# Performance work log

Hardware: AMD Instinct MI355X
Metric: run time of the kernel (lower is better)

## Reference

```python
import jax, jax.numpy as jnp
import numpy as np

N = 50000      # amino-acid nodes
DIN = 64       # input feature dim
DH = 64        # hidden dim (= GAT out_feats per head)
H = 4          # attention heads
E_RES, E_SEQ, E_KNN = 400000, 100000, 400000
EPS = 1e-5


def setup_inputs() -> dict:
    key = jax.random.key(0)
    ks = iter(jax.random.split(key, 32))
    def nrm(shape, scale=0.1):
        return jax.random.normal(next(ks), shape, dtype=jnp.float32) * scale
    def edges(E):
        s = jax.random.randint(next(ks), (E,), 0, N, dtype=jnp.int32)
        d = jax.random.randint(next(ks), (E,), 0, N, dtype=jnp.int32)
        return s, d
    x = nrm((N, DIN), 1.0)
    src_res, dst_res = edges(E_RES)
    src_seq, dst_seq = edges(E_SEQ)
    src_knn, dst_knn = edges(E_KNN)
    inp = dict(x=x, src_res=src_res, dst_res=dst_res, src_seq=src_seq,
               dst_seq=dst_seq, src_knn=src_knn, dst_knn=dst_knn)
    # layer 0 (in=DIN), layer 1 (in=DH): per-relation stacked GAT params
    inp.update(W0=nrm((3, DIN, H * DH)), al0=nrm((3, H, DH)), ar0=nrm((3, H, DH)),
               b0=nrm((3, H * DH)), rW0=nrm((3, DIN, H * DH)))
    inp.update(W1=nrm((3, DH, H * DH)), al1=nrm((3, H, DH)), ar1=nrm((3, H, DH)),
               b1=nrm((3, H * DH)), rW1=nrm((3, DH, H * DH)))
    inp.update(fcW0=nrm((DH, DH)), fcb0=nrm((DH,)), fcW1=nrm((DH, DH)), fcb1=nrm((DH,)))
    inp.update(g0=jnp.ones((DIN,), jnp.float32), be0=jnp.zeros((DIN,), jnp.float32),
               g1=jnp.ones((DH,), jnp.float32), be1=jnp.zeros((DH,), jnp.float32))
    return inp


def _bn(x, g, b):
    mu = jnp.mean(x, axis=0)
    var = jnp.mean((x - mu) ** 2, axis=0)
    return (x - mu) * jax.lax.rsqrt(var + EPS) * g + b


def _gat(h, src, dst, W, al, ar, bias, rW):
    # DGL GATConv (feat_drop off in eval, residual=True via res_fc Linear, bias)
    n = h.shape[0]
    fs = (h @ W).reshape(n, H, DH)                    # [N,H,D]
    el = jnp.sum(fs * al, axis=-1)                    # [N,H]
    er = jnp.sum(fs * ar, axis=-1)
    e = jax.nn.leaky_relu(el[src] + er[dst], 0.2)     # [E,H]
    m = jax.ops.segment_max(e, dst, num_segments=n)
    a = jnp.exp(e - m[dst])
    s = jax.ops.segment_sum(a, dst, num_segments=n)
    alpha = a / s[dst]                                # edge-softmax per dst/head
    rst = jax.ops.segment_sum(alpha[:, :, None] * fs[src], dst, num_segments=n)
    return rst + (h @ rW).reshape(n, H, DH) + bias.reshape(1, H, DH)


def _layer(x, edges, W, al, ar, b, rW, fcW, fcb, g, be):
    x = _bn(x, g, be)
    h = jnp.zeros((x.shape[0], H, DH), x.dtype)
    for r, (s_, d_) in enumerate(edges):              # 3 relation types, summed
        h = h + _gat(x, s_, d_, W[r], al[r], ar[r], b[r], rW[r])
    x = jnp.mean(h, axis=1)                           # mean over heads
    return jax.nn.relu(x @ fcW + fcb)


def reference(x, src_res, dst_res, src_seq, dst_seq, src_knn, dst_knn,
              W0, al0, ar0, b0, rW0, W1, al1, ar1, b1, rW1,
              fcW0, fcb0, fcW1, fcb1, g0, be0, g1, be1):
    edges = [(src_res, dst_res), (src_seq, dst_seq), (src_knn, dst_knn)]
    x = _layer(x, edges, W0, al0, ar0, b0, rW0, fcW0, fcb0, g0, be0)
    x = _layer(x, edges, W1, al1, ar1, b1, rW1, fcW1, fcb1, g1, be1)
    return x
```

## Files before the change

kernel.cpp:

```cpp
#include <hip/hip_runtime.h>
#include <math.h>

#define NN    50000
#define DD    64
#define HH    4
#define E_RES 400000
#define E_SEQ 100000
#define E_KNN 400000
#define ETOT  (E_RES+E_SEQ+E_KNN)
#define RPS   (NN + 4)
#define NBLK  ((NN+255)/256)
#define KTOT  864
#define CTPS  (ETOT + 32)
#define NBUK  98
#define TBUK  (3*NBUK)
#define EPB   4096
#define PABLK ((ETOT+EPB-1)/EPB)
#define FBLK  (NN/16)
#define ECB2  ((3*NN + 31)/32)
#define LZS   810

typedef __attribute__((ext_vector_type(8))) short short8;
typedef __attribute__((ext_vector_type(4))) float floatx4;

__device__ inline unsigned short f2bf(float f){
  union{float f; unsigned u;} v; v.f=f;
  unsigned r = v.u + 0x7FFF + ((v.u>>16)&1);
  return (unsigned short)(r>>16);
}
__device__ inline float bf2f(unsigned short u){
  union{unsigned u; float f;} v; v.u=(unsigned)u<<16; return v.f;
}

__global__ void __launch_bounds__(256)
k_bucketcnt(const int* __restrict__ d0, const int* __restrict__ d1,
            const int* __restrict__ d2, int* __restrict__ bcnt){
  __shared__ int cnt[TBUK];
  int t = threadIdx.x;
  for(int i=t;i<TBUK;i+=256) cnt[i]=0;
  __syncthreads();
  int ebase = blockIdx.x*EPB;
  #pragma unroll
  for(int j=0;j<16;j++){
    int i = ebase + j*256 + t;
    int d, r;
    if(i < E_RES){ d=d0[i]; r=0; }
    else if(i < E_RES+E_SEQ){ d=d1[i-E_RES]; r=1; }
    else if(i < ETOT){ d=d2[i-E_RES-E_SEQ]; r=2; }
    else continue;
    atomicAdd(&cnt[r*NBUK + (d>>9)], 1);
  }
  __syncthreads();
  for(int i=t;i<TBUK;i+=256){ int c=cnt[i]; if(c) atomicAdd(&bcnt[i], c); }
}

__global__ void k_bucketscan(const int* __restrict__ bcnt,
                             int* __restrict__ bbase, int* __restrict__ bcur){
  __shared__ int sh[TBUK];
  int t = threadIdx.x;
  if(t < 64){
    int carry = 0;
    for(int c=0;c<5;c++){
      int idx = c*64 + t;
      int v = (idx < TBUK) ? bcnt[idx] : 0;
      int inc = v;
      for(int off=1; off<64; off<<=1){ int n=__shfl_up(inc, off, 64); if(t>=off) inc+=n; }
      if(idx < TBUK) sh[idx] = carry + inc - v;
      carry += __shfl(inc, 63, 64);
    }
  }
  __syncthreads();
  if(t < TBUK){ bbase[t] = sh[t]; bcur[t] = sh[t]; }
  if(t == 0) bbase[TBUK] = ETOT;
}

__global__ void __launch_bounds__(256)
k_partA(const int* __restrict__ s0, const int* __restrict__ d0,
        const int* __restrict__ s1, const int* __restrict__ d1,
        const int* __restrict__ s2, const int* __restrict__ d2,
        int* __restrict__ bcur, unsigned* __restrict__ pairs){
  __shared__ int cnt[TBUK];
  __shared__ int gb[TBUK];
  int t = threadIdx.x;
  for(int i=t;i<TBUK;i+=256) cnt[i]=0;
  __syncthreads();
  int ebase = blockIdx.x*EPB;
  unsigned meta[16], pk[16];
  #pragma unroll
  for(int j=0;j<16;j++){
    int i = ebase + j*256 + t;
    int s, d, r;
    if(i < E_RES){ s=s0[i]; d=d0[i]; r=0; }
    else if(i < E_RES+E_SEQ){ int k=i-E_RES; s=s1[k]; d=d1[k]; r=1; }
    else if(i < ETOT){ int k=i-E_RES-E_SEQ; s=s2[k]; d=d2[k]; r=2; }
    else { meta[j]=0xFFFFFFFFu; continue; }
    int bk = r*NBUK + (d>>9);
    int rk = atomicAdd(&cnt[bk], 1);
    meta[j] = ((unsigned)bk<<16) | (unsigned)rk;
    pk[j]   = ((unsigned)(d&511)<<16) | (unsigned)s;
  }
  __syncthreads();
  for(int i=t;i<TBUK;i+=256){ int c=cnt[i]; gb[i] = c ? atomicAdd(&bcur[i], c) : 0; }
  __syncthreads();
  #pragma unroll
  for(int j=0;j<16;j++){
    unsigned mt = meta[j];
    if(mt != 0xFFFFFFFFu)
      pairs[gb[mt>>16] + (mt & 0xFFFFu)] = pk[j];
  }
}

__global__ void __launch_bounds__(256)
k_partB(const unsigned* __restrict__ pairs, const int* __restrict__ bbase,
        int* __restrict__ rowptr, int* __restrict__ csr){
  int bb = blockIdx.x, r = bb / NBUK, b = bb - r*NBUK;
  int dbase = b*512, dmax = min(512, NN - dbase);
  int off = (r==0)?0:(r==1)?E_RES:(E_RES+E_SEQ);
  __shared__ int hist[512];
  __shared__ int curs[513];
  int t = threadIdx.x;
  hist[t]=0; hist[256+t]=0;
  __syncthreads();
  int beg = bbase[bb], end = bbase[bb+1];
  for(int i=beg+t; i<end; i+=256) atomicAdd(&hist[pairs[i]>>16], 1);
  __syncthreads();
  if(t < 64){
    int carry = 0;
    for(int c=0;c<8;c++){
      int v = hist[c*64+t];
      int inc = v;
      for(int o2=1; o2<64; o2<<=1){ int n=__shfl_up(inc, o2, 64); if(t>=o2) inc+=n; }
      curs[c*64+t] = (beg - off) + carry + inc - v;
      carry += __shfl(inc, 63, 64);
    }
    if(t==0) curs[512] = end - off;
  }
  __syncthreads();
  int* rp = rowptr + r*RPS + dbase;
  for(int i=t; i<=dmax; i+=256) rp[i] = curs[i];
  __syncthreads();
  for(int i=beg+t; i<end; i+=256){
    unsigned p = pairs[i];
    int pos = atomicAdd(&curs[p>>16], 1);
    csr[off + pos] = (int)(p & 0xFFFFu);
  }
}

__global__ void k_bnstats(const float* __restrict__ x, float* __restrict__ stats,
                          unsigned short* __restrict__ Abf){
  __shared__ float sh[512];
  int t = threadIdx.x, col = t & 63, rg = t >> 6;
  float s=0.f, q=0.f;
  for(int row = blockIdx.x*4 + rg; row < NN; row += gridDim.x*4){
    float v = x[(size_t)row*64 + col]; s += v; q += v*v;
    Abf[(size_t)row*64 + col] = f2bf(v);
  }
  sh[t]=s; sh[256+t]=q; __syncthreads();
  if(rg==0){
    s = sh[col]+sh[64+col]+sh[128+col]+sh[192+col];
    q = sh[256+col]+sh[320+col]+sh[384+col]+sh[448+col];
    atomicAdd(&stats[col], s); atomicAdd(&stats[64+col], q);
  }
}

__global__ void __launch_bounds__(256)
k_prep3(const float* __restrict__ stats, const float* __restrict__ g,
        const float* __restrict__ be, const float* __restrict__ W,
        const float* __restrict__ al, const float* __restrict__ ar,
        const float* __restrict__ b, const float* __restrict__ rW,
        const float* __restrict__ fcW, const float* __restrict__ fcb,
        float* __restrict__ wbufF){
  __shared__ float scale[64], shift[64];
  int t = threadIdx.x;
  if(t<64){
    float mu  = stats[t]*(1.0f/NN);
    float var = stats[64+t]*(1.0f/NN) - mu*mu;
    float sc  = g[t]*rsqrtf(var + 1e-5f);
    scale[t]=sc; shift[t]=be[t]-mu*sc;
  }
  __syncthreads();
  char* wb = (char*)wbufF;
  unsigned short* Wf = (unsigned short*)wbufF;
  float* biasF = (float*)(wb + 110592);
  int bid = blockIdx.x;
  if(bid < 52){
    __shared__ float fcWs[4096];
    for(int i=t;i<4096;i+=256) fcWs[i]=fcW[i];
    __syncthreads();
    int j = bid*16 + (t>>4);
    int cg = (t&15)*4;
    float Wrow[64];
    if(j < 64){
      for(int d=0; d<64; d++){
        float w=0.f;
        for(int r=0;r<3;r++)
          #pragma unroll
          for(int h=0;h<4;h++)
            w += rW[((size_t)(r*64+j))*256 + h*64 + d];
        Wrow[d] = scale[j]*0.25f*w;
      }
    } else {
      int jj = j-64;
      int r = jj>>8, dc = jj&255, h = dc&3, c = dc>>2;
      const float* Wp = W + ((size_t)(r*64+c))*256 + h*64;
      float sc = 0.25f*scale[c];
      #pragma unroll
      for(int d=0; d<64; d++) Wrow[d] = sc*Wp[d];
    }
    #pragma unroll
    for(int cc=0; cc<4; cc++){
      int col = cg+cc;
      float acc=0.f;
      #pragma unroll
      for(int d=0; d<64; d++) acc += Wrow[d]*fcWs[d*64+col];
      Wf[(size_t)col*KTOT + j] = f2bf(acc);
    }
  } else if(bid < 58){
    int wv = (bid-52)*4 + (t>>6);
    int r = wv >> 3, cc = wv & 7, h = cc & 3, k = t & 63;
    const float* av = ((cc>=4)?ar:al) + (r*HH+h)*64;
    const float* Wk = W + ((size_t)(r*64+k))*256 + h*64;
    float w=0.f;
    for(int d2=0; d2<64; d2++) w += Wk[d2]*av[d2];
    float* WelR = (float*)(wb + 110848 + r*2080);
    WelR[cc*64 + k] = scale[k]*w;
    float bp = shift[k]*w;
    for(int off=32; off; off>>=1) bp += __shfl_down(bp, off, 64);
    if(k==0) (WelR + 512)[cc] = bp;
  } else {
    __shared__ float S[3][64];
    __shared__ float BH[64];
    if(t<192){
      int r=t>>6, d=t&63;
      float s=0.f;
      #pragma unroll
      for(int h=0;h<4;h++){
        const float* Wp = W + (size_t)(r*64)*256 + h*64 + d;
        for(int k=0;k<64;k++) s += shift[k]*Wp[(size_t)k*256];
      }
      S[r][d]=0.25f*s;
    } else {
      int d = t-192;
      float s=0.f;
      for(int k=0;k<64;k++){
        float w=0.f;
        for(int r=0;r<3;r++)
          #pragma unroll
          for(int h=0;h<4;h++)
            w += rW[((size_t)(r*64+k))*256 + h*64 + d];
        s += shift[k]*0.25f*w;
      }
      float bb=0.f;
      for(int r=0;r<3;r++)
        #pragma unroll
        for(int h=0;h<4;h++) bb += b[r*256 + h*64 + d];
      BH[d] = s + 0.25f*bb;
    }
    __syncthreads();
    if(t<192){
      int r=t>>6, col=t&63;
      float acc=0.f;
      for(int d=0;d<64;d++) acc += S[r][d]*fcW[d*64+col];
      Wf[(size_t)col*KTOT + 832 + r] = f2bf(acc);
    } else {
      int col=t-192;
      float acc=0.f;
      for(int d=0;d<64;d++) acc += BH[d]*fcW[d*64+col];
      biasF[col] = acc + fcb[col];
    }
    if(t<64){
      for(int j=835;j<KTOT;j++) Wf[(size_t)t*KTOT + j] = 0;
    }
  }
}

__global__ void __launch_bounds__(256)
k_el3(const float* __restrict__ A, const float* __restrict__ wbufF,
      float* __restrict__ EL){
  int r = blockIdx.x / NBLK;
  const char* wb = (const char*)wbufF;
  const float* Wel = (const float*)(wb + 110848 + r*2080);
  const float* biasE = Wel + 512;
  float* ELr = EL + (size_t)r*NN*8;
  __shared__ float sw[512];
  __shared__ float sb[8];
  int t = threadIdx.x;
  sw[t]=Wel[t]; sw[256+t]=Wel[256+t];
  if(t<8) sb[t]=biasE[t];
  __syncthreads();
  int n = (blockIdx.x % NBLK)*256 + t;
  if(n>=NN) return;
  float acc[8];
  #pragma unroll
  for(int c=0;c<8;c++) acc[c]=sb[c];
  const float4* Ar = (const float4*)(A + (size_t)n*64);
  #pragma unroll
  for(int kq=0;kq<16;kq++){
    float4 a = Ar[kq];
    #pragma unroll
    for(int c=0;c<8;c++){
      const float* w = sw + c*64 + kq*4;
      acc[c] += a.x*w[0] + a.y*w[1] + a.z*w[2] + a.w*w[3];
    }
  }
  ((float4*)ELr)[n*2]   = make_float4(acc[0],acc[1],acc[2],acc[3]);
  ((float4*)ELr)[n*2+1] = make_float4(acc[4],acc[5],acc[6],acc[7]);
}

#define EC_GATHER(ii, E0,E1,E2,E3) { \
    int src_ = cs[ii]; \
    float4 el_ = ((const float4*)ELr)[src_*2]; \
    E0=el_.x+er.x; E1=el_.y+er.y; E2=el_.z+er.z; E3=el_.w+er.w; \
    E0 = E0>0.f? E0 : 0.2f*E0; \
    E1 = E1>0.f? E1 : 0.2f*E1; \
    E2 = E2>0.f? E2 : 0.2f*E2; \
    E3 = E3>0.f? E3 : 0.2f*E3; }
#define EC_ACC(E0,E1,E2,E3) { \
    float n0_=fmaxf(m0,E0); s0=s0*__expf(m0-n0_)+__expf(E0-n0_); m0=n0_; \
    float n1_=fmaxf(m1,E1); s1=s1*__expf(m1-n1_)+__expf(E1-n1_); m1=n1_; \
    float n2_=fmaxf(m2,E2); s2=s2*__expf(m2-n2_)+__expf(E2-n2_); m2=n2_; \
    float n3_=fmaxf(m3,E3); s3=s3*__expf(m3-n3_)+__expf(E3-n3_); m3=n3_; }
#define EC_COMB(o) { \
    float om_,os_,nm_; \
    om_=__shfl_xor(m0,o,64); os_=__shfl_xor(s0,o,64); \
    nm_=fmaxf(m0,om_); s0=s0*__expf(m0-nm_)+os_*__expf(om_-nm_); m0=nm_; \
    om_=__shfl_xor(m1,o,64); os_=__shfl_xor(s1,o,64); \
    nm_=fmaxf(m1,om_); s1=s1*__expf(m1-nm_)+os_*__expf(om_-nm_); m1=nm_; \
    om_=__shfl_xor(m2,o,64); os_=__shfl_xor(s2,o,64); \
    nm_=fmaxf(m2,om_); s2=s2*__expf(m2-nm_)+os_*__expf(om_-nm_); m2=nm_; \
    om_=__shfl_xor(m3,o,64); os_=__shfl_xor(s3,o,64); \
    nm_=fmaxf(m3,om_); s3=s3*__expf(m3-nm_)+os_*__expf(om_-nm_); m3=nm_; }
#define EC_STORE(ii, E0,E1,E2,E3) { \
    t0[ii]=f2bf(__expf(E0-m0)*r0); t1[ii]=f2bf(__expf(E1-m1)*r1); \
    t2[ii]=f2bf(__expf(E2-m2)*r2); t3[ii]=f2bf(__expf(E3-m3)*r3); }

__global__ void __launch_bounds__(256)
k_edgecoef3(const float* __restrict__ EL, const int* __restrict__ rowptr,
            const int* __restrict__ csr, unsigned short* __restrict__ coefT){
  int item = blockIdx.x*32 + (threadIdx.x>>3);
  int sl = threadIdx.x & 7;
  if(item >= 3*NN) return;
  int r = item / NN, n = item - r*NN;
  const float* ELr = EL + (size_t)r*NN*8;
  const int* rp = rowptr + r*RPS;
  int off = (r==0)?0:(r==1)?E_RES:(E_RES+E_SEQ);
  const int* cs = csr + off;
  unsigned short* t0 = coefT + off;
  unsigned short* t1 = coefT + (size_t)CTPS + off;
  unsigned short* t2 = coefT + (size_t)2*CTPS + off;
  unsigned short* t3 = coefT + (size_t)3*CTPS + off;
  int beg = rp[n], end = rp[n+1];
  if(end <= beg) return;
  const float4 er = ((const float4*)ELr)[n*2+1];
  float m0=-1e30f,m1=-1e30f,m2=-1e30f,m3=-1e30f;
  float s0=0.f,s1=0.f,s2=0.f,s3=0.f;
  int i0 = beg + sl, i1 = i0 + 8, i2 = i0 + 16, i3 = i0 + 24;
  bool h0 = i0 < end, h1 = i1 < end, h2 = i2 < end, h3 = i3 < end;
  float a0=0.f,a1=0.f,a2=0.f,a3=0.f;
  float b0=0.f,b1=0.f,b2=0.f,b3=0.f;
  float c0=0.f,c1=0.f,c2=0.f,c3=0.f;
  float d0=0.f,d1=0.f,d2=0.f,d3=0.f;
  if(h0){ EC_GATHER(i0, a0,a1,a2,a3); EC_ACC(a0,a1,a2,a3); }
  if(h1){ EC_GATHER(i1, b0,b1,b2,b3); EC_ACC(b0,b1,b2,b3); }
  if(h2){ EC_GATHER(i2, c0,c1,c2,c3); EC_ACC(c0,c1,c2,c3); }
  if(h3){ EC_GATHER(i3, d0,d1,d2,d3); EC_ACC(d0,d1,d2,d3); }
  for(int i = i0 + 32; i < end; i += 8){
    float e0,e1,e2,e3;
    EC_GATHER(i, e0,e1,e2,e3);
    EC_ACC(e0,e1,e2,e3);
  }
  EC_COMB(1) EC_COMB(2) EC_COMB(4)
  float r0=1.f/s0, r1=1.f/s1, r2=1.f/s2, r3=1.f/s3;
  if(h0) EC_STORE(i0, a0,a1,a2,a3);
  if(h1) EC_STORE(i1, b0,b1,b2,b3);
  if(h2) EC_STORE(i2, c0,c1,c2,c3);
  if(h3) EC_STORE(i3, d0,d1,d2,d3);
  for(int i = i0 + 32; i < end; i += 8){
    float e0,e1,e2,e3;
    EC_GATHER(i, e0,e1,e2,e3);
    EC_STORE(i, e0,e1,e2,e3);
  }
}

__global__ void __launch_bounds__(256)
k_fused(const unsigned short* __restrict__ Abf, const int* __restrict__ rowptr,
        const int* __restrict__ csr, const unsigned short* __restrict__ coefT,
        const float* __restrict__ wbufF, float* __restrict__ out,
        unsigned short* __restrict__ Abf2, float* __restrict__ stats, int dostats){
  __shared__ unsigned short Zl[16*LZS];
  const unsigned short* Wf = (const unsigned short*)wbufF;
  const float* biasF = (const float*)((const char*)wbufF + 110592);
  int t = threadIdx.x, wv = t>>6, lane = t&63, m = lane&15, kq = lane>>4;
  int nb = blockIdx.x*16;
  int n4 = nb + wv*4;
  int nn = m>>2, h = m&3;
  for(int i=t; i<512; i+=256){ int nd=i>>5, j=i&31; if(j<29) Zl[nd*LZS+771+j]=0; }
  for(int r=0;r<3;r++){
    const int* rp = rowptr + r*RPS;
    int off = (r==0)?0:(r==1)?E_RES:(E_RES+E_SEQ);
    const int* cs = csr + off;
    const unsigned short* cT = coefT + (size_t)h*CTPS + off;
    int rpn  = rp[n4+nn];
    int rpn1 = rp[n4+nn+1];
    unsigned dg = (unsigned)(rpn1 - rpn);
    int beg = __shfl(rpn, 0, 64);
    int end = __shfl(rpn1, 15, 64);
    floatx4 acc0={0.f,0.f,0.f,0.f};
    floatx4 acc1={0.f,0.f,0.f,0.f};
    floatx4 acc2={0.f,0.f,0.f,0.f};
    floatx4 acc3={0.f,0.f,0.f,0.f};
    for(int eb = (beg & ~31); eb < end; eb += 32){
      int p0 = eb + kq*8;
      union { uint4 q; short8 v; } af;
      af.q = *(const uint4*)(cT + p0);
      int qd = p0 - rpn;
      unsigned w0 = (((unsigned)(qd+0)<dg)?0x0000FFFFu:0u) | (((unsigned)(qd+1)<dg)?0xFFFF0000u:0u);
      unsigned w1 = (((unsigned)(qd+2)<dg)?0x0000FFFFu:0u) | (((unsigned)(qd+3)<dg)?0xFFFF0000u:0u);
      unsigned w2 = (((unsigned)(qd+4)<dg)?0x0000FFFFu:0u) | (((unsigned)(qd+5)<dg)?0xFFFF0000u:0u);
      unsigned w3 = (((unsigned)(qd+6)<dg)?0x0000FFFFu:0u) | (((unsigned)(qd+7)<dg)?0xFFFF0000u:0u);
      af.q.x &= w0; af.q.y &= w1; af.q.z &= w2; af.q.w &= w3;
      const int* csp = cs + p0;
      int s0=csp[0],s1=csp[1],s2=csp[2],s3=csp[3],s4=csp[4],s5=csp[5],s6=csp[6],s7=csp[7];
      const unsigned short* q0 = Abf + ((size_t)s0<<6) + m;
      const unsigned short* q1 = Abf + ((size_t)s1<<6) + m;
      const unsigned short* q2 = Abf + ((size_t)s2<<6) + m;
      const unsigned short* q3 = Abf + ((size_t)s3<<6) + m;
      const unsigned short* q4 = Abf + ((size_t)s4<<6) + m;
      const unsigned short* q5 = Abf + ((size_t)s5<<6) + m;
      const unsigned short* q6 = Abf + ((size_t)s6<<6) + m;
      const unsigned short* q7 = Abf + ((size_t)s7<<6) + m;
      union { unsigned u[4]; short8 v; } b0,b1,b2,b3;
      b0.u[0]=(unsigned)q0[0] |((unsigned)q1[0]<<16);
      b0.u[1]=(unsigned)q2[0] |((unsigned)q3[0]<<16);
      b0.u[2]=(unsigned)q4[0] |((unsigned)q5[0]<<16);
      b0.u[3]=(unsigned)q6[0] |((unsigned)q7[0]<<16);
      b1.u[0]=(unsigned)q0[16]|((unsigned)q1[16]<<16);
      b1.u[1]=(unsigned)q2[16]|((unsigned)q3[16]<<16);
      b1.u[2]=(unsigned)q4[16]|((unsigned)q5[16]<<16);
      b1.u[3]=(unsigned)q6[16]|((unsigned)q7[16]<<16);
      b2.u[0]=(unsigned)q0[32]|((unsigned)q1[32]<<16);
      b2.u[1]=(unsigned)q2[32]|((unsigned)q3[32]<<16);
      b2.u[2]=(unsigned)q4[32]|((unsigned)q5[32]<<16);
      b2.u[3]=(unsigned)q6[32]|((unsigned)q7[32]<<16);
      b3.u[0]=(unsigned)q0[48]|((unsigned)q1[48]<<16);
      b3.u[1]=(unsigned)q2[48]|((unsigned)q3[48]<<16);
      b3.u[2]=(unsigned)q4[48]|((unsigned)q5[48]<<16);
      b3.u[3]=(unsigned)q6[48]|((unsigned)q7[48]<<16);
      acc0 = __builtin_amdgcn_mfma_f32_16x16x32_bf16(af.v, b0.v, acc0, 0,0,0);
      acc1 = __builtin_amdgcn_mfma_f32_16x16x32_bf16(af.v, b1.v, acc1, 0,0,0);
      acc2 = __builtin_amdgcn_mfma_f32_16x16x32_bf16(af.v, b2.v, acc2, 0,0,0);
      acc3 = __builtin_amdgcn_mfma_f32_16x16x32_bf16(af.v, b3.v, acc3, 0,0,0);
    }
    unsigned short* zrow = Zl + (wv*4+kq)*LZS + r*256 + m*4;
    ushort4 o;
    o.x=f2bf(acc0[0]); o.y=f2bf(acc0[1]); o.z=f2bf(acc0[2]); o.w=f2bf(acc0[3]);
    *(ushort4*)(zrow)       = o;
    o.x=f2bf(acc1[0]); o.y=f2bf(acc1[1]); o.z=f2bf(acc1[2]); o.w=f2bf(acc1[3]);
    *(ushort4*)(zrow + 64)  = o;
    o.x=f2bf(acc2[0]); o.y=f2bf(acc2[1]); o.z=f2bf(acc2[2]); o.w=f2bf(acc2[3]);
    *(ushort4*)(zrow + 128) = o;
    o.x=f2bf(acc3[0]); o.y=f2bf(acc3[1]); o.z=f2bf(acc3[2]); o.w=f2bf(acc3[3]);
    *(ushort4*)(zrow + 192) = o;
    int degk = __shfl((int)dg, kq<<2, 64);
    if(m==0)
      Zl[(wv*4+kq)*LZS + 768 + r] = degk>0 ? (unsigned short)0x3F80 : (unsigned short)0;
  }
  __syncthreads();
  floatx4 acc = {0.f,0.f,0.f,0.f};
  const unsigned short* Arow = Abf + (size_t)(nb+m)*64;
  const unsigned short* Zrow = Zl + m*LZS;
  #pragma unroll
  for(int kb=0; kb<27; kb++){
    short8 a;
    if(kb<2) a = *(const short8*)(Arow + kb*32 + kq*8);
    else     a = *(const short8*)(Zrow + (kb-2)*32 + kq*8);
    short8 b = *(const short8*)(Wf + (size_t)(wv*16+m)*KTOT + kb*32 + kq*8);
    acc = __builtin_amdgcn_mfma_f32_16x16x32_bf16(a, b, acc, 0,0,0);
  }
  int col = wv*16 + m;
  float bb = biasF[col];
  float sv=0.f, qv=0.f;
  #pragma unroll
  for(int ri=0; ri<4; ri++){
    int ro = nb + kq*4 + ri;
    float v = fmaxf(acc[ri] + bb, 0.f);
    out[(size_t)ro*64 + col] = v;
    if(dostats){
      Abf2[(size_t)ro*64 + col] = f2bf(v);
      sv += v; qv += v*v;
    }
  }
  if(dostats){
    sv += __shfl_xor(sv, 16, 64); qv += __shfl_xor(qv, 16, 64);
    sv += __shfl_xor(sv, 32, 64); qv += __shfl_xor(qv, 32, 64);
    if(kq==0){ atomicAdd(&stats[col], sv); atomicAdd(&stats[64+col], qv); }
  }
}

extern "C" void kernel_launch(void* const* d_in, const int* in_sizes, int n_in,
                              void* d_out, int out_size, void* d_ws, size_t ws_size,
                              hipStream_t stream){
  const float* x      =(const float*)d_in[0];
  const int* src_res  =(const int*)d_in[1];
  const int* dst_res  =(const int*)d_in[2];
  const int* src_seq  =(const int*)d_in[3];
  const int* dst_seq  =(const int*)d_in[4];
  const int* src_knn  =(const int*)d_in[5];
  const int* dst_knn  =(const int*)d_in[6];
  const float* W0 =(const float*)d_in[7];
  const float* al0=(const float*)d_in[8];
  const float* ar0=(const float*)d_in[9];
  const float* b0 =(const float*)d_in[10];
  const float* rW0=(const float*)d_in[11];
  const float* W1 =(const float*)d_in[12];
  const float* al1=(const float*)d_in[13];
  const float* ar1=(const float*)d_in[14];
  const float* b1 =(const float*)d_in[15];
  const float* rW1=(const float*)d_in[16];
  const float* fcW0=(const float*)d_in[17];
  const float* fcb0=(const float*)d_in[18];
  const float* fcW1=(const float*)d_in[19];
  const float* fcb1=(const float*)d_in[20];
  const float* g0 =(const float*)d_in[21];
  const float* be0=(const float*)d_in[22];
  const float* g1 =(const float*)d_in[23];
  const float* be1=(const float*)d_in[24];

  char* ws=(char*)d_ws;
  int*   bcnt   =(int*)  (ws+0);
  int*   bbase  =(int*)  (ws+4096);
  float* stats0 =(float*)(ws+600000);
  float* stats1 =(float*)(ws+600512);
  int*   rowptr =(int*)  (ws+601024);
  int*   bcur   =(int*)  (ws+1201088);
  int*   csr    =(int*)  (ws+1801088);
  float* wbuf   =(float*)(ws+5401088);
  unsigned short* Abf  =(unsigned short*)(ws+5526528);
  unsigned* pairs =(unsigned*)(ws+27000000UL);
  float* xbuf   =(float*)(ws+91926528UL);
  float* EL     =(float*)(ws+104726528UL);
  unsigned short* coefT=(unsigned short*)(ws+109526528UL);
  unsigned short* Abf2 =(unsigned short*)(ws+123926528UL);

  hipMemsetAsync(ws, 0, 601024, stream);

  k_bucketcnt<<<PABLK,256,0,stream>>>(dst_res,dst_seq,dst_knn,bcnt);
  k_bucketscan<<<1,512,0,stream>>>(bcnt,bbase,bcur);
  k_partA<<<PABLK,256,0,stream>>>(src_res,dst_res,src_seq,dst_seq,
                                  src_knn,dst_knn,bcur,pairs);
  k_partB<<<TBUK,256,0,stream>>>(pairs,bbase,rowptr,csr);

  k_bnstats<<<256,256,0,stream>>>(x,stats0,Abf);
  k_prep3<<<59,256,0,stream>>>(stats0,g0,be0,W0,al0,ar0,b0,rW0,fcW0,fcb0,wbuf);
  k_el3<<<3*NBLK,256,0,stream>>>(x,wbuf,EL);
  k_edgecoef3<<<ECB2,256,0,stream>>>(EL,rowptr,csr,coefT);
  k_fused<<<FBLK,256,0,stream>>>(Abf,rowptr,csr,coefT,wbuf,xbuf,Abf2,stats1,1);
  k_prep3<<<59,256,0,stream>>>(stats1,g1,be1,W1,al1,ar1,b1,rW1,fcW1,fcb1,wbuf);
  k_el3<<<3*NBLK,256,0,stream>>>(xbuf,wbuf,EL);
  k_edgecoef3<<<ECB2,256,0,stream>>>(EL,rowptr,csr,coefT);
  k_fused<<<FBLK,256,0,stream>>>(Abf2,rowptr,csr,coefT,wbuf,(float*)d_out,Abf2,stats0,0);
}
```

Measured before the change: 409.0 us.

## Widen prep3 weight-fold parallelism and batch gather loads ahead of MFMA

The weight-folding part of k_prep3 is spread over 208 blocks instead of 52. Each thread now computes one output column through a shared-memory row buffer, which replaces the per-thread 64-float register row, so the launch grows to 215 blocks. In k_fused, all 32 gathered bf16 loads are issued together before the mask computation, so more memory requests are in flight at once, and launch_bounds adds a minimum-occupancy hint of 4. The trade-off is more blocks re-reading fcW into shared memory, and possible register pressure or spills from the gather batching under the occupancy cap.

```diff
diff --git a/kernel.cpp b/kernel.cpp
--- a/kernel.cpp
+++ b/kernel.cpp
@@ -183,40 +183,36 @@
   unsigned short* Wf = (unsigned short*)wbufF;
   float* biasF = (float*)(wb + 110592);
   int bid = blockIdx.x;
-  if(bid < 52){
+  if(bid < 208){
     __shared__ float fcWs[4096];
+    __shared__ float WrowS[4][64];
     for(int i=t;i<4096;i+=256) fcWs[i]=fcW[i];
-    __syncthreads();
-    int j = bid*16 + (t>>4);
-    int cg = (t&15)*4;
-    float Wrow[64];
-    if(j < 64){
-      for(int d=0; d<64; d++){
+    int jg = t>>6, col = t&63;
+    int j = bid*4 + jg;
+    {
+      int d = col;
+      float wr;
+      if(j < 64){
         float w=0.f;
         for(int r=0;r<3;r++)
           #pragma unroll
           for(int h=0;h<4;h++)
             w += rW[((size_t)(r*64+j))*256 + h*64 + d];
-        Wrow[d] = scale[j]*0.25f*w;
+        wr = scale[j]*0.25f*w;
+      } else {
+        int jj = j-64;
+        int r = jj>>8, dc = jj&255, h = dc&3, c = dc>>2;
+        wr = 0.25f*scale[c]*W[((size_t)(r*64+c))*256 + h*64 + d];
       }
-    } else {
-      int jj = j-64;
-      int r = jj>>8, dc = jj&255, h = dc&3, c = dc>>2;
-      const float* Wp = W + ((size_t)(r*64+c))*256 + h*64;
-      float sc = 0.25f*scale[c];
-      #pragma unroll
-      for(int d=0; d<64; d++) Wrow[d] = sc*Wp[d];
-    }
+      WrowS[jg][d] = wr;
+    }
+    __syncthreads();
+    float acc=0.f;
     #pragma unroll
-    for(int cc=0; cc<4; cc++){
-      int col = cg+cc;
-      float acc=0.f;
-      #pragma unroll
-      for(int d=0; d<64; d++) acc += Wrow[d]*fcWs[d*64+col];
-      Wf[(size_t)col*KTOT + j] = f2bf(acc);
-    }
-  } else if(bid < 58){
-    int wv = (bid-52)*4 + (t>>6);
+    for(int d=0; d<64; d++) acc += WrowS[jg][d]*fcWs[d*64+col];
+    Wf[(size_t)col*KTOT + j] = f2bf(acc);
+  } else if(bid < 214){
+    int wv = (bid-208)*4 + (t>>6);
     int r = wv >> 3, cc = wv & 7, h = cc & 3, k = t & 63;
     const float* av = ((cc>=4)?ar:al) + (r*HH+h)*64;
     const float* Wk = W + ((size_t)(r*64+k))*256 + h*64;
@@ -382,7 +378,7 @@
   }
 }
 
-__global__ void __launch_bounds__(256)
+__global__ void __launch_bounds__(256, 4)
 k_fused(const unsigned short* __restrict__ Abf, const int* __restrict__ rowptr,
         const int* __restrict__ csr, const unsigned short* __restrict__ coefT,
         const float* __restrict__ wbufF, float* __restrict__ out,
@@ -413,39 +409,30 @@
       int p0 = eb + kq*8;
       union { uint4 q; short8 v; } af;
       af.q = *(const uint4*)(cT + p0);
+      const int* csp = cs + p0;
+      int sr[8];
+      #pragma unroll
+      for(int j=0;j<8;j++) sr[j] = csp[j];
+      unsigned va[8][4];
+      #pragma unroll
+      for(int j=0;j<8;j++){
+        const unsigned short* q = Abf + ((size_t)sr[j]<<6) + m;
+        va[j][0]=q[0]; va[j][1]=q[16]; va[j][2]=q[32]; va[j][3]=q[48];
+      }
       int qd = p0 - rpn;
       unsigned w0 = (((unsigned)(qd+0)<dg)?0x0000FFFFu:0u) | (((unsigned)(qd+1)<dg)?0xFFFF0000u:0u);
       unsigned w1 = (((unsigned)(qd+2)<dg)?0x0000FFFFu:0u) | (((unsigned)(qd+3)<dg)?0xFFFF0000u:0u);
       unsigned w2 = (((unsigned)(qd+4)<dg)?0x0000FFFFu:0u) | (((unsigned)(qd+5)<dg)?0xFFFF0000u:0u);
       unsigned w3 = (((unsigned)(qd+6)<dg)?0x0000FFFFu:0u) | (((unsigned)(qd+7)<dg)?0xFFFF0000u:0u);
       af.q.x &= w0; af.q.y &= w1; af.q.z &= w2; af.q.w &= w3;
-      const int* csp = cs + p0;
-      int s0=csp[0],s1=csp[1],s2=csp[2],s3=csp[3],s4=csp[4],s5=csp[5],s6=csp[6],s7=csp[7];
-      const unsigned short* q0 = Abf + ((size_t)s0<<6) + m;
-      const unsigned short* q1 = Abf + ((size_t)s1<<6) + m;
-      const unsigned short* q2 = Abf + ((size_t)s2<<6) + m;
-      const unsigned short* q3 = Abf + ((size_t)s3<<6) + m;
-      const unsigned short* q4 = Abf + ((size_t)s4<<6) + m;
-      const unsigned short* q5 = Abf + ((size_t)s5<<6) + m;
-      const unsigned short* q6 = Abf + ((size_t)s6<<6) + m;
-      const unsigned short* q7 = Abf + ((size_t)s7<<6) + m;
       union { unsigned u[4]; short8 v; } b0,b1,b2,b3;
-      b0.u[0]=(unsigned)q0[0] |((unsigned)q1[0]<<16);
-      b0.u[1]=(unsigned)q2[0] |((unsigned)q3[0]<<16);
-      b0.u[2]=(unsigned)q4[0] |((unsigned)q5[0]<<16);
-      b0.u[3]=(unsigned)q6[0] |((unsigned)q7[0]<<16);
-      b1.u[0]=(unsigned)q0[16]|((unsigned)q1[16]<<16);
-      b1.u[1]=(unsigned)q2[16]|((unsigned)q3[16]<<16);
-      b1.u[2]=(unsigned)q4[16]|((unsigned)q5[16]<<16);
-      b1.u[3]=(unsigned)q6[16]|((unsigned)q7[16]<<16);
-      b2.u[0]=(unsigned)q0[32]|((unsigned)q1[32]<<16);
-      b2.u[1]=(unsigned)q2[32]|((unsigned)q3[32]<<16);
-      b2.u[2]=(unsigned)q4[32]|((unsigned)q5[32]<<16);
-      b2.u[3]=(unsigned)q6[32]|((unsigned)q7[32]<<16);
-      b3.u[0]=(unsigned)q0[48]|((unsigned)q1[48]<<16);
-      b3.u[1]=(unsigned)q2[48]|((unsigned)q3[48]<<16);
-      b3.u[2]=(unsigned)q4[48]|((unsigned)q5[48]<<16);
-      b3.u[3]=(unsigned)q6[48]|((unsigned)q7[48]<<16);
+      #pragma unroll
+      for(int k=0;k<4;k++){
+        b0.u[k] = va[2*k][0] | (va[2*k+1][0]<<16);
+        b1.u[k] = va[2*k][1] | (va[2*k+1][1]<<16);
+        b2.u[k] = va[2*k][2] | (va[2*k+1][2]<<16);
+        b3.u[k] = va[2*k][3] | (va[2*k+1][3]<<16);
+      }
       acc0 = __builtin_amdgcn_mfma_f32_16x16x32_bf16(af.v, b0.v, acc0, 0,0,0);
       acc1 = __builtin_amdgcn_mfma_f32_16x16x32_bf16(af.v, b1.v, acc1, 0,0,0);
       acc2 = __builtin_amdgcn_mfma_f32_16x16x32_bf16(af.v, b2.v, acc2, 0,0,0);
@@ -551,11 +538,11 @@
   k_partB<<<TBUK,256,0,stream>>>(pairs,bbase,rowptr,csr);
 
   k_bnstats<<<256,256,0,stream>>>(x,stats0,Abf);
-  k_prep3<<<59,256,0,stream>>>(stats0,g0,be0,W0,al0,ar0,b0,rW0,fcW0,fcb0,wbuf);
+  k_prep3<<<215,256,0,stream>>>(stats0,g0,be0,W0,al0,ar0,b0,rW0,fcW0,fcb0,wbuf);
   k_el3<<<3*NBLK,256,0,stream>>>(x,wbuf,EL);
   k_edgecoef3<<<ECB2,256,0,stream>>>(EL,rowptr,csr,coefT);
   k_fused<<<FBLK,256,0,stream>>>(Abf,rowptr,csr,coefT,wbuf,xbuf,Abf2,stats1,1);
-  k_prep3<<<59,256,0,stream>>>(stats1,g1,be1,W1,al1,ar1,b1,rW1,fcW1,fcb1,wbuf);
+  k_prep3<<<215,256,0,stream>>>(stats1,g1,be1,W1,al1,ar1,b1,rW1,fcW1,fcb1,wbuf);
   k_el3<<<3*NBLK,256,0,stream>>>(xbuf,wbuf,EL);
   k_edgecoef3<<<ECB2,256,0,stream>>>(EL,rowptr,csr,coefT);
   k_fused<<<FBLK,256,0,stream>>>(Abf2,rowptr,csr,coefT,wbuf,(float*)d_out,Abf2,stats0,0);
```

Result: slower. 455.3 us (+11.3%).
